# Kernel optimization log

Hardware: AMD Instinct MI355X
Metric: run time of the kernel (lower is better)

## Reference

```python
import jax, jax.numpy as jnp
import numpy as np
import math

B, S, D, H = 4, 2048, 1024, 16
HD = D // H  # 64

def setup_inputs() -> dict:
    key = jax.random.key(0)
    ks = jax.random.split(key, 4)
    x = jax.random.normal(ks[0], (B, S, D), dtype=jnp.float32)
    # causal mask, True = attend (precomputed as in the original usage)
    mask = jnp.tril(jnp.ones((S, S), dtype=bool))[None, None, :, :]
    c_attn_w = jax.random.normal(ks[1], (D, 3 * D), dtype=jnp.float32) * 0.02
    c_attn_b = jnp.zeros((3 * D,), dtype=jnp.float32)
    c_proj_w = jax.random.normal(ks[2], (D, D), dtype=jnp.float32) * 0.02
    c_proj_b = jnp.zeros((D,), dtype=jnp.float32)
    return {"x": x, "mask": mask, "c_attn_w": c_attn_w, "c_attn_b": c_attn_b,
            "c_proj_w": c_proj_w, "c_proj_b": c_proj_b}

def reference(x, mask, c_attn_w, c_attn_b, c_proj_w, c_proj_b):
    b, s, d = x.shape
    # c_attn: Conv1D acts as Linear with transposed weight convention
    qkv = x @ c_attn_w + c_attn_b                      # [B,S,3D]
    q, k, v = jnp.split(qkv, 3, axis=-1)
    q = q.reshape(b, s, H, HD).transpose(0, 2, 1, 3)   # [B,H,S,hd]
    k = k.reshape(b, s, H, HD).transpose(0, 2, 1, 3)   # [B,H,S,hd]
    v = v.reshape(b, s, H, HD).transpose(0, 2, 1, 3)   # [B,H,S,hd]
    # scores, scale by sqrt(head_dim) (done unconditionally in _attn)
    w = jnp.einsum('bhqd,bhkd->bhqk', q, k) / math.sqrt(HD)
    # masked_fill_(1 - mask, -10000.0)
    w = jnp.where(mask, w, jnp.float32(-10000.0))
    w = jax.nn.softmax(w, axis=-1)                     # attn_dropout p=0
    a = jnp.einsum('bhqk,bhkd->bhqd', w, v)            # [B,H,S,hd]
    a = a.transpose(0, 2, 1, 3).reshape(b, s, d)       # merge heads
    out = a @ c_proj_w + c_proj_b                      # resid_dropout p=0
    return out
```

## Files before the change

kernel.cpp:

```cpp
#include <hip/hip_runtime.h>

#define SEQ  2048
#define DIM  1024
#define NH   16
#define HD   64
#define NB   4

typedef __bf16 bf16_t;
typedef bf16_t bf16x8 __attribute__((ext_vector_type(8)));
typedef bf16_t bf16x4 __attribute__((ext_vector_type(4)));
typedef float  floatx4 __attribute__((ext_vector_type(4)));

#define MFMA16(a, b, c) __builtin_amdgcn_mfma_f32_16x16x32_bf16((a), (b), (c), 0, 0, 0)

__device__ __forceinline__ void gl_lds16(const bf16_t* g, bf16_t* l) {
    __builtin_amdgcn_global_load_lds(
        (const __attribute__((address_space(1))) void*)g,
        (__attribute__((address_space(3))) void*)l,
        16, 0, 0);
}

__global__ __launch_bounds__(256) void prep(
    const float* __restrict__ x, bf16_t* __restrict__ xb,
    const float* __restrict__ wqkv, bf16_t* __restrict__ wqkvT,
    const float* __restrict__ wproj, bf16_t* __restrict__ wprojT) {
    const int bid = blockIdx.x, tid = threadIdx.x;
    if (bid < 8192) {
        const int i = (bid * 256 + tid) * 4;
        const float4 v = *(const float4*)(x + i);
        xb[i + 0] = (bf16_t)v.x;
        xb[i + 1] = (bf16_t)v.y;
        xb[i + 2] = (bf16_t)v.z;
        xb[i + 3] = (bf16_t)v.w;
        return;
    }
    __shared__ bf16_t t[32][33];
    const float* in;
    bf16_t* out;
    int R, C, bx, by;
    if (bid < 8192 + 3072) {
        const int idx = bid - 8192;
        in = wqkv; out = wqkvT; R = 1024; C = 3072;
        bx = idx % 96; by = idx / 96;
    } else {
        const int idx = bid - 11264;
        in = wproj; out = wprojT; R = 1024; C = 1024;
        bx = idx & 31; by = idx >> 5;
    }
    const int c0 = bx * 32, r0 = by * 32;
    const int tx = tid & 31, ty = tid >> 5;
#pragma unroll
    for (int i = 0; i < 32; i += 8)
        t[ty + i][tx] = (bf16_t)in[(r0 + ty + i) * C + c0 + tx];
    __syncthreads();
#pragma unroll
    for (int i = 0; i < 32; i += 8)
        out[(c0 + ty + i) * R + r0 + tx] = t[tx][ty + i];
}

template <int MODE>
__global__ __launch_bounds__(256, 2) void gemm128(
    const bf16_t* __restrict__ A, const bf16_t* __restrict__ Bt,
    const float* __restrict__ bias, int K,
    bf16_t* __restrict__ Qo, bf16_t* __restrict__ Ko, bf16_t* __restrict__ Vo,
    float* __restrict__ Co) {
    __shared__ __align__(16) bf16_t smem[MODE == 0 ? 128 * 136 : 128 * 128];
    bf16_t* Al = smem;
    bf16_t* Bl = smem + 128 * 64;

    const int tid = threadIdx.x;
    const int m0 = blockIdx.y * 128, n0 = blockIdx.x * 128;
    const int w = tid >> 6, lane = tid & 63;
    const int l15 = lane & 15, quad = lane >> 4;
    const int wm = (w & 1) * 64, wn = (w >> 1) * 64;

    floatx4 acc[4][4] = {};

    const int g_st = ((tid & 7) - (tid >> 3)) & 7;
    const bf16_t* aptr = A + (m0 + (tid >> 3)) * K + g_st * 8;
    const bf16_t* bptr = Bt + (n0 + (tid >> 3)) * K + g_st * 8;
    bf16_t* al = Al + tid * 8;
    bf16_t* bl = Bl + tid * 8;

    for (int k0 = 0; k0 < K; k0 += 64) {
#pragma unroll
        for (int c = 0; c < 4; c++) {
            gl_lds16(aptr + (c * 32) * K, al + c * 2048);
            gl_lds16(bptr + (c * 32) * K, bl + c * 2048);
        }
        aptr += 64;
        bptr += 64;
        __syncthreads();

#pragma unroll
        for (int h = 0; h < 2; h++) {
            const int sAB = (((h << 2) + quad + (l15 & 7)) & 7) * 8;
            bf16x8 af[4], bfr[4];
#pragma unroll
            for (int i = 0; i < 4; i++)
                af[i] = *(const bf16x8*)&Al[(wm + i * 16 + l15) * 64 + sAB];
#pragma unroll
            for (int j = 0; j < 4; j++)
                bfr[j] = *(const bf16x8*)&Bl[(wn + j * 16 + l15) * 64 + sAB];
#pragma unroll
            for (int i = 0; i < 4; i++)
#pragma unroll
                for (int j = 0; j < 4; j++)
                    acc[i][j] = MODE == 0 ? MFMA16(bfr[j], af[i], acc[i][j])
                                          : MFMA16(af[i], bfr[j], acc[i][j]);
        }
        __syncthreads();
    }

    if (MODE == 0) {
        bf16_t* Cl = smem;
        const int which = n0 >> 10;
        const float qs = (which == 0) ? 0.18033688f : 1.0f;
#pragma unroll
        for (int j = 0; j < 4; j++) {
            const int nc = wn + j * 16 + quad * 4;
#pragma unroll
            for (int i = 0; i < 4; i++) {
                const int mrow = wm + i * 16 + l15;
                bf16x4 pk;
#pragma unroll
                for (int r = 0; r < 4; r++)
                    pk[r] = (bf16_t)((acc[i][j][r] + bias[n0 + nc + r]) * qs);
                *(bf16x4*)&Cl[mrow * 136 + nc] = pk;
            }
        }
        __syncthreads();

        if (which < 2) {
            const int row = tid >> 1, ch = (tid & 1) << 6;
            const int m = m0 + row, b = m >> 11, s = m & 2047;
            const int h = ((n0 & 1023) >> 6) + (ch >> 6);
            bf16_t* dst = (which == 0 ? Qo : Ko) + ((size_t)(b * NH + h) * SEQ + s) * HD;
            const bf16_t* src = Cl + row * 136 + ch;
#pragma unroll
            for (int g = 0; g < 8; g++)
                *(bf16x8*)(dst + g * 8) = *(const bf16x8*)(src + g * 8);
        } else {
            const int dl = tid & 127, sh = (tid >> 7) << 6;
            const int h = ((n0 & 1023) >> 6) + (dl >> 6), d = dl & 63;
            const int b = m0 >> 11, sbase = (m0 & 2047) + sh;
            bf16_t* dst = Vo + ((size_t)(b * NH + h) * HD + d) * SEQ + sbase;
#pragma unroll
            for (int g = 0; g < 8; g++) {
                bf16x8 tv;
#pragma unroll
                for (int e = 0; e < 8; e++)
                    tv[e] = Cl[(sh + g * 8 + e) * 136 + dl];
                *(bf16x8*)(dst + g * 8) = tv;
            }
        }
    } else {
#pragma unroll
        for (int j = 0; j < 4; j++) {
            const int n = n0 + wn + j * 16 + l15;
            const float bv = bias[n];
#pragma unroll
            for (int i = 0; i < 4; i++)
#pragma unroll
                for (int r = 0; r < 4; r++) {
                    const int m = m0 + wm + i * 16 + quad * 4 + r;
                    Co[m * 1024 + n] = acc[i][j][r] + bv;
                }
        }
    }
}

__global__ __launch_bounds__(256, 4) void attn64(
    const bf16_t* __restrict__ Q, const bf16_t* __restrict__ Kg,
    const bf16_t* __restrict__ Vt, bf16_t* __restrict__ Aout) {
    __shared__ __align__(16) bf16_t Ks[2 * 64 * 64];
    __shared__ __align__(16) bf16_t Vs[2 * 64 * 64];
    __shared__ __align__(16) bf16_t Ps[64 * 64];

    const int bh = blockIdx.x;
    const int qt = 15 - (blockIdx.y >> 1);
    const int hb = 1 - (blockIdx.y & 1);
    const int qbase0 = qt * 128 + hb * 64;
    const int nk = 2 * qt + hb + 1;

    const int tid = threadIdx.x, w = tid >> 6, lane = tid & 63;
    const int l15 = lane & 15, quad = lane >> 4;
    const int b = bh >> 4, hd = bh & 15;
    const int xk = l15 & 7;

    bf16x8 aq[2];
    {
        const bf16_t* qr = Q + (size_t)(bh * SEQ + qbase0 + w * 16 + l15) * HD;
#pragma unroll
        for (int h = 0; h < 2; h++)
            aq[h] = *(const bf16x8*)(qr + h * 32 + quad * 8);
    }

    floatx4 o[4] = {};
    float li = 0.f;

    const int srow = tid >> 3;
    const int sg = (tid & 7) ^ (srow & 7);
    const bf16_t* kgl = Kg + (size_t)bh * SEQ * HD + (size_t)srow * HD + sg * 8;
    const bf16_t* vgl = Vt + (size_t)bh * HD * SEQ + (size_t)srow * SEQ + sg * 8;

    auto stage = [&](int buf, int kt) {
        const bf16_t* kp = kgl + kt * (64 * HD);
        const bf16_t* vp = vgl + kt * 64;
        bf16_t* kd = Ks + buf * 4096 + tid * 8;
        bf16_t* vd = Vs + buf * 4096 + tid * 8;
        gl_lds16(kp, kd);
        gl_lds16(kp + 32 * HD, kd + 2048);
        gl_lds16(vp, vd);
        gl_lds16(vp + 32 * SEQ, vd + 2048);
    };

    auto proc = [&](int kt, int buf) {
        const bf16_t* Ksub = Ks + buf * 4096;
        const bf16_t* Vsub = Vs + buf * 4096;
        bf16x8 bk[4][2];
#pragma unroll
        for (int j = 0; j < 4; j++) {
            const int n = j * 16 + l15;
#pragma unroll
            for (int h = 0; h < 2; h++)
                bk[j][h] = *(const bf16x8*)&Ksub[n * 64 + (((h * 4 + quad) ^ xk) * 8)];
        }
        floatx4 z[4] = {};
        __builtin_amdgcn_s_setprio(1);
#pragma unroll
        for (int j = 0; j < 4; j++) {
            z[j] = MFMA16(bk[j][0], aq[0], z[j]);
            z[j] = MFMA16(bk[j][1], aq[1], z[j]);
        }
        __builtin_amdgcn_s_setprio(0);
        {
            const int qbase = qbase0 + w * 16;
            const int qrow_l = qbase + l15;
            const bool full = (kt * 64 + 63) <= qbase;
            const int prow = w * 16 + l15;
            bf16_t* pbase = Ps + prow * 64;
            const int rx = prow & 7;
#pragma unroll
            for (int j = 0; j < 4; j++) {
                const int kg0 = kt * 64 + j * 16 + quad * 4;
                bf16x4 pk;
                float es[4];
#pragma unroll
                for (int r = 0; r < 4; r++) {
                    float e = __builtin_amdgcn_exp2f(z[j][r]);
                    if (!full && kg0 + r > qrow_l) e = 0.f;
                    es[r] = e;
                    pk[r] = (bf16_t)e;
                }
                li += (es[0] + es[1]) + (es[2] + es[3]);
                const int g = 2 * j + (quad >> 1);
                *(bf16x4*)(pbase + (((g ^ rx) << 3) | ((quad & 1) << 2))) = pk;
            }
        }
        __builtin_amdgcn_s_waitcnt(0xC07F);
        bf16x8 ap[2];
        {
            const int row = w * 16 + l15;
#pragma unroll
            for (int kk = 0; kk < 2; kk++)
                ap[kk] = *(const bf16x8*)&Ps[row * 64 +
                                            (((kk * 4 + quad) ^ (row & 7)) << 3)];
        }
        bf16x8 bv[4][2];
#pragma unroll
        for (int j = 0; j < 4; j++) {
            const int n = j * 16 + l15;
#pragma unroll
            for (int kk = 0; kk < 2; kk++)
                bv[j][kk] = *(const bf16x8*)&Vsub[n * 64 + (((kk * 4 + quad) ^ xk) * 8)];
        }
        __builtin_amdgcn_s_setprio(1);
#pragma unroll
        for (int j = 0; j < 4; j++) {
            o[j] = MFMA16(ap[0], bv[j][0], o[j]);
            o[j] = MFMA16(ap[1], bv[j][1], o[j]);
        }
        __builtin_amdgcn_s_setprio(0);
    };

    stage(0, 0);
    __syncthreads();
    for (int kt = 0; kt < nk; ++kt) {
        const int cur = kt & 1;
        if (kt + 1 < nk) stage(cur ^ 1, kt + 1);
        proc(kt, cur);
        __syncthreads();
    }

    {
        float s = li;
        s += __shfl_xor(s, 16, 64);
        s += __shfl_xor(s, 32, 64);
#pragma unroll
        for (int r = 0; r < 4; r++) {
            const float sv = __shfl(s, quad * 4 + r, 64);
            const float inv = 1.0f / sv;
            const int srow_o = qbase0 + w * 16 + quad * 4 + r;
            bf16_t* orow = Aout + (size_t)(b * SEQ + srow_o) * DIM + hd * HD;
#pragma unroll
            for (int j = 0; j < 4; j++)
                orow[j * 16 + l15] = (bf16_t)(o[j][r] * inv);
        }
    }
}

extern "C" void kernel_launch(void* const* d_in, const int* in_sizes, int n_in,
                              void* d_out, int out_size, void* d_ws, size_t ws_size,
                              hipStream_t stream) {
    const float* x        = (const float*)d_in[0];
    const float* c_attn_w = (const float*)d_in[2];
    const float* c_attn_b = (const float*)d_in[3];
    const float* c_proj_w = (const float*)d_in[4];
    const float* c_proj_b = (const float*)d_in[5];
    float* out = (float*)d_out;

    char* ws = (char*)d_ws;
    bf16_t* xb     = (bf16_t*)ws; ws += (size_t)NB * SEQ * DIM * 2;
    bf16_t* wqkvT  = (bf16_t*)ws; ws += (size_t)3072 * 1024 * 2;
    bf16_t* wprojT = (bf16_t*)ws; ws += (size_t)1024 * 1024 * 2;
    bf16_t* Qb  = (bf16_t*)ws; ws += (size_t)NB * NH * SEQ * HD * 2;
    bf16_t* Kb  = (bf16_t*)ws; ws += (size_t)NB * NH * SEQ * HD * 2;
    bf16_t* Vtb = (bf16_t*)ws; ws += (size_t)NB * NH * SEQ * HD * 2;
    bf16_t* Ab  = (bf16_t*)ws; ws += (size_t)NB * SEQ * DIM * 2;

    prep<<<12288, 256, 0, stream>>>(x, xb, c_attn_w, wqkvT, c_proj_w, wprojT);

    gemm128<0><<<dim3(24, 64), 256, 0, stream>>>(xb, wqkvT, c_attn_b, 1024,
                                                 Qb, Kb, Vtb, nullptr);

    attn64<<<dim3(NB * NH, 32), 256, 0, stream>>>(Qb, Kb, Vtb, Ab);

    gemm128<1><<<dim3(8, 64), 256, 0, stream>>>(Ab, wprojT, c_proj_b, 1024,
                                                nullptr, nullptr, nullptr, out);
}
```

Baseline: 267.4 us.

## Split attention tile work across waves by key columns instead of query rows

Each wave now holds Q fragments for all 64 query rows and takes a 16-key slice of the K tile for the score MFMAs. For the PV product it takes a 16-column slice of the head dimension and reads the full P tile from LDS. The goal is fewer per-wave LDS reads of K and V fragments, at the cost of more P reads, an extra block-wide barrier inside every key tile, and four times the Q register footprint. Row sums are now partial per wave and are combined through LDS before normalising the output.

```diff
diff --git a/kernel.cpp b/kernel.cpp
--- a/kernel.cpp
+++ b/kernel.cpp
@@ -188,16 +188,17 @@
     const int b = bh >> 4, hd = bh & 15;
     const int xk = l15 & 7;
 
-    bf16x8 aq[2];
-    {
-        const bf16_t* qr = Q + (size_t)(bh * SEQ + qbase0 + w * 16 + l15) * HD;
-#pragma unroll
-        for (int h = 0; h < 2; h++)
-            aq[h] = *(const bf16x8*)(qr + h * 32 + quad * 8);
+    bf16x8 aq[4][2];
+#pragma unroll
+    for (int j = 0; j < 4; j++) {
+        const bf16_t* qr = Q + (size_t)(bh * SEQ + qbase0 + j * 16 + l15) * HD;
+#pragma unroll
+        for (int kk = 0; kk < 2; kk++)
+            aq[j][kk] = *(const bf16x8*)(qr + kk * 32 + quad * 8);
     }
 
     floatx4 o[4] = {};
-    float li = 0.f;
+    float lip[4] = {};
 
     const int srow = tid >> 3;
     const int sg = (tid & 7) ^ (srow & 7);
@@ -218,68 +219,62 @@
     auto proc = [&](int kt, int buf) {
         const bf16_t* Ksub = Ks + buf * 4096;
         const bf16_t* Vsub = Vs + buf * 4096;
-        bf16x8 bk[4][2];
-#pragma unroll
-        for (int j = 0; j < 4; j++) {
-            const int n = j * 16 + l15;
-#pragma unroll
-            for (int h = 0; h < 2; h++)
-                bk[j][h] = *(const bf16x8*)&Ksub[n * 64 + (((h * 4 + quad) ^ xk) * 8)];
-        }
+        bf16x8 ak[2];
+        const int krow = w * 16 + l15;
+#pragma unroll
+        for (int kk = 0; kk < 2; kk++)
+            ak[kk] = *(const bf16x8*)&Ksub[krow * 64 + (((kk * 4 + quad) ^ xk) * 8)];
         floatx4 z[4] = {};
         __builtin_amdgcn_s_setprio(1);
 #pragma unroll
         for (int j = 0; j < 4; j++) {
-            z[j] = MFMA16(bk[j][0], aq[0], z[j]);
-            z[j] = MFMA16(bk[j][1], aq[1], z[j]);
+            z[j] = MFMA16(ak[0], aq[j][0], z[j]);
+            z[j] = MFMA16(ak[1], aq[j][1], z[j]);
         }
         __builtin_amdgcn_s_setprio(0);
-        {
-            const int qbase = qbase0 + w * 16;
-            const int qrow_l = qbase + l15;
-            const bool full = (kt * 64 + 63) <= qbase;
-            const int prow = w * 16 + l15;
-            bf16_t* pbase = Ps + prow * 64;
-            const int rx = prow & 7;
-#pragma unroll
-            for (int j = 0; j < 4; j++) {
-                const int kg0 = kt * 64 + j * 16 + quad * 4;
-                bf16x4 pk;
-                float es[4];
-#pragma unroll
-                for (int r = 0; r < 4; r++) {
-                    float e = __builtin_amdgcn_exp2f(z[j][r]);
-                    if (!full && kg0 + r > qrow_l) e = 0.f;
-                    es[r] = e;
-                    pk[r] = (bf16_t)e;
-                }
-                li += (es[0] + es[1]) + (es[2] + es[3]);
-                const int g = 2 * j + (quad >> 1);
-                *(bf16x4*)(pbase + (((g ^ rx) << 3) | ((quad & 1) << 2))) = pk;
+        const int kg0 = kt * 64 + w * 16 + quad * 4;
+        const int kmax = kt * 64 + w * 16 + 15;
+#pragma unroll
+        for (int j = 0; j < 4; j++) {
+            const bool full = kmax <= (qbase0 + j * 16);
+            const int q_l = j * 16 + l15;
+            const int qabs = qbase0 + q_l;
+            bf16x4 pk;
+            float es[4];
+#pragma unroll
+            for (int r = 0; r < 4; r++) {
+                float e = __builtin_amdgcn_exp2f(z[j][r]);
+                if (!full && kg0 + r > qabs) e = 0.f;
+                es[r] = e;
+                pk[r] = (bf16_t)e;
             }
-        }
-        __builtin_amdgcn_s_waitcnt(0xC07F);
-        bf16x8 ap[2];
-        {
-            const int row = w * 16 + l15;
-#pragma unroll
-            for (int kk = 0; kk < 2; kk++)
-                ap[kk] = *(const bf16x8*)&Ps[row * 64 +
-                                            (((kk * 4 + quad) ^ (row & 7)) << 3)];
-        }
-        bf16x8 bv[4][2];
-#pragma unroll
-        for (int j = 0; j < 4; j++) {
-            const int n = j * 16 + l15;
-#pragma unroll
-            for (int kk = 0; kk < 2; kk++)
-                bv[j][kk] = *(const bf16x8*)&Vsub[n * 64 + (((kk * 4 + quad) ^ xk) * 8)];
+            lip[j] += (es[0] + es[1]) + (es[2] + es[3]);
+            const int gs = (w * 2 + (quad >> 1)) ^ (q_l & 7);
+            *(bf16x4*)&Ps[q_l * 64 + gs * 8 + (quad & 1) * 4] = pk;
+        }
+        bf16x8 bv[2];
+        const int vrow = w * 16 + l15;
+#pragma unroll
+        for (int kk = 0; kk < 2; kk++)
+            bv[kk] = *(const bf16x8*)&Vsub[vrow * 64 + (((kk * 4 + quad) ^ xk) * 8)];
+        asm volatile("s_waitcnt lgkmcnt(0)" ::: "memory");
+        __builtin_amdgcn_s_barrier();
+        asm volatile("" ::: "memory");
+        bf16x8 ap[4][2];
+#pragma unroll
+        for (int i = 0; i < 4; i++) {
+            const int q_l = i * 16 + l15;
+#pragma unroll
+            for (int kk = 0; kk < 2; kk++) {
+                const int gs = (kk * 4 + quad) ^ (q_l & 7);
+                ap[i][kk] = *(const bf16x8*)&Ps[q_l * 64 + gs * 8];
+            }
         }
         __builtin_amdgcn_s_setprio(1);
 #pragma unroll
-        for (int j = 0; j < 4; j++) {
-            o[j] = MFMA16(ap[0], bv[j][0], o[j]);
-            o[j] = MFMA16(ap[1], bv[j][1], o[j]);
+        for (int i = 0; i < 4; i++) {
+            o[i] = MFMA16(ap[i][0], bv[0], o[i]);
+            o[i] = MFMA16(ap[i][1], bv[1], o[i]);
         }
         __builtin_amdgcn_s_setprio(0);
     };
@@ -293,19 +288,31 @@
         __syncthreads();
     }
 
+    float* liL = (float*)Ps;
+    float* inv = liL + 256;
     {
-        float s = li;
-        s += __shfl_xor(s, 16, 64);
-        s += __shfl_xor(s, 32, 64);
+#pragma unroll
+        for (int j = 0; j < 4; j++) {
+            float s = lip[j];
+            s += __shfl_xor(s, 16, 64);
+            s += __shfl_xor(s, 32, 64);
+            if (quad == 0) liL[w * 64 + j * 16 + l15] = s;
+        }
+    }
+    __syncthreads();
+    if (w == 0) {
+        const float s = liL[lane] + liL[64 + lane] + liL[128 + lane] + liL[192 + lane];
+        inv[lane] = 1.0f / s;
+    }
+    __syncthreads();
+#pragma unroll
+    for (int i = 0; i < 4; i++) {
 #pragma unroll
         for (int r = 0; r < 4; r++) {
-            const float sv = __shfl(s, quad * 4 + r, 64);
-            const float inv = 1.0f / sv;
-            const int srow_o = qbase0 + w * 16 + quad * 4 + r;
-            bf16_t* orow = Aout + (size_t)(b * SEQ + srow_o) * DIM + hd * HD;
-#pragma unroll
-            for (int j = 0; j < 4; j++)
-                orow[j * 16 + l15] = (bf16_t)(o[j][r] * inv);
+            const int q_l = i * 16 + quad * 4 + r;
+            const float iv = inv[q_l];
+            Aout[(size_t)(b * SEQ + qbase0 + q_l) * DIM + hd * HD + w * 16 + l15] =
+                (bf16_t)(o[i][r] * iv);
         }
     }
 }
```

After: 269.8 us. About the same (+0.9%).
